# Kernel tuning notes

Measured on AMD Instinct MI355X. Metric: run time of the kernel, lower is better.

Reference implementation:

```python
import jax, jax.numpy as jnp
import numpy as np

B, LT, D, H, DI = 8, 128, 512, 8, 2048
NMEM, LMEM = 1024, 64
DH = D // H
EPS = 1e-5
NEG = -1e9

def _ln(x, g, b):
    mu = x.mean(-1, keepdims=True)
    var = ((x - mu) ** 2).mean(-1, keepdims=True)
    return (x - mu) * jax.lax.rsqrt(var + EPS) * g + b

def _ffn(x, W1, b1, W2, b2):
    # PositionwiseFF with residual=True (dropout=0 / eval)
    return x + jax.nn.relu(x @ W1 + b1) @ W2 + b2

def setup_inputs():
    key = jax.random.key(0)
    ks = jax.random.split(key, 16)
    w = lambda i, shape: jax.random.normal(ks[i], shape, jnp.float32) * 0.02
    return {
        "dec_output": jax.random.normal(ks[0], (B, LT, D), jnp.float32),
        "mem_attn_out": jax.random.normal(ks[1], (B, LT, NMEM + 1), jnp.float32),
        "enc_out_mem": jax.random.normal(ks[2], (NMEM, LMEM, D), jnp.float32),
        "tgt_emb_mem": jax.random.normal(ks[3], (NMEM, LMEM, D), jnp.float32),
        "tgt_mask_mem": jax.random.randint(ks[4], (NMEM, LMEM), 0, 2, jnp.int32),
        "tgt_mask": jax.random.randint(ks[5], (B, LT), 0, 2, jnp.int32),
        "g0": jnp.ones((D,), jnp.float32), "be0": jnp.zeros((D,), jnp.float32),
        "g1": jnp.ones((D,), jnp.float32), "be1": jnp.zeros((D,), jnp.float32),
        "Wq": w(6, (D, D)), "bq": jnp.zeros((D,), jnp.float32),
        "Wk": w(7, (D, D)), "bk": jnp.zeros((D,), jnp.float32),
        "Wv": w(8, (D, D)), "bv": jnp.zeros((D,), jnp.float32),
        "Wo": w(9, (D, D)), "bo": jnp.zeros((D,), jnp.float32),
        "f1W1": w(10, (D, DI)), "f1b1": jnp.zeros((DI,), jnp.float32),
        "f1W2": w(11, (DI, D)), "f1b2": jnp.zeros((D,), jnp.float32),
        "f2W1": w(12, (D, DI)), "f2b1": jnp.zeros((DI,), jnp.float32),
        "f2W2": w(13, (DI, D)), "f2b2": jnp.zeros((D,), jnp.float32),
    }

def reference(dec_output, mem_attn_out, enc_out_mem, tgt_emb_mem, tgt_mask_mem, tgt_mask,
              g0, be0, g1, be1, Wq, bq, Wk, bk, Wv, bv, Wo, bo,
              f1W1, f1b1, f1W2, f1b2, f2W1, f2b1, f2W2, f2b2):
    x = _ln(dec_output, g0, be0)                       # [B,LT,D]
    N = B * LT
    samples = jnp.argmax(mem_attn_out, -1).reshape(N) - 1   # [-1, NMEM-1]
    valid = samples >= 0                               # [N]
    s = jnp.maximum(samples, 0)                        # clamp; masked later
    q = x.reshape(N, 1, D)
    # gather memory per selected query (torch compacts via unique; same math)
    k_in = enc_out_mem[s]                              # [N,LMEM,D]
    v_in = tgt_emb_mem[s]                              # [N,LMEM,D]
    kmask = tgt_mask_mem[s] != 0                       # True = valid key
    # multi-head attention, residual=True
    qh = (q @ Wq + bq).reshape(N, 1, H, DH).transpose(0, 2, 1, 3)     # [N,H,1,DH]
    kh = (k_in @ Wk + bk).reshape(N, LMEM, H, DH).transpose(0, 2, 1, 3)
    vh = (v_in @ Wv + bv).reshape(N, LMEM, H, DH).transpose(0, 2, 1, 3)
    scores = jnp.einsum('nhqd,nhkd->nhqk', qh, kh) / (DH ** 0.5)      # [N,H,1,LMEM]
    scores = jnp.where(kmask[:, None, None, :], scores, NEG)
    attn = jax.nn.softmax(scores, axis=-1)
    ctx = jnp.einsum('nhqk,nhkd->nhqd', attn, vh).transpose(0, 2, 1, 3).reshape(N, 1, D)
    st = q + ctx @ Wo + bo
    st = _ffn(st, f1W1, f1b1, f1W2, f1b2)
    st = _ln(st, g1, be1)
    # scatter back: positions with sample == -1 get zeros
    st = jnp.where(valid[:, None, None], st, 0.0)
    dec = x + st.reshape(B, LT, D)
    dec = _ffn(dec, f2W1, f2b1, f2W2, f2b2)
    return dec
```

## Files before the change

kernel.cpp:

```cpp
#include <hip/hip_runtime.h>
#include <math.h>

#define NQ   1024
#define DIM  512
#define NH   8
#define DHD  64
#define DFF  2048
#define LM   64

typedef __bf16 bf16x8 __attribute__((ext_vector_type(8)));
typedef float  f32x4  __attribute__((ext_vector_type(4)));

__device__ __forceinline__ unsigned short f2bf(float f) {
    unsigned u = __builtin_bit_cast(unsigned, f);
    return (unsigned short)((u + 0x7fffu + ((u >> 16) & 1u)) >> 16);
}
__device__ __forceinline__ float bflo(unsigned p) {
    return __builtin_bit_cast(float, p << 16);
}
__device__ __forceinline__ float bfhi(unsigned p) {
    return __builtin_bit_cast(float, p & 0xffff0000u);
}

__device__ __forceinline__ void gload16(const void* g, void* l) {
    __builtin_amdgcn_global_load_lds(
        (const __attribute__((address_space(1))) unsigned*)g,
        (__attribute__((address_space(3))) unsigned*)l, 16, 0, 0);
}

__device__ __forceinline__ float blk_sum(float v, volatile float* red) {
#pragma unroll
    for (int o = 32; o; o >>= 1) v += __shfl_down(v, o);
    __syncthreads();
    if ((threadIdx.x & 63) == 0) red[threadIdx.x >> 6] = v;
    __syncthreads();
    return red[0] + red[1] + red[2] + red[3];
}

struct PrepPtrs {
    const float* src[8];
    unsigned short* dst[8];
};
__global__ __launch_bounds__(256) void prep_ln0_k(
    PrepPtrs p,
    const float* __restrict__ dec_out, const float* __restrict__ attn_out,
    const float* __restrict__ g, const float* __restrict__ be,
    float* __restrict__ x, unsigned* __restrict__ xb, int* __restrict__ samples)
{
    __shared__ float tile[32][33];
    __shared__ float red[4];
    __shared__ float rv[4]; __shared__ int ri[4];
    const int bid = blockIdx.x;

    if (bid < 5120) {
        int m, lt;
        if (bid < 1024) { m = bid >> 8; lt = bid & 255; }
        else { m = 4 + ((bid - 1024) >> 10); lt = (bid - 1024) & 1023; }
        const int RS = (m < 4) ? 512 : ((m == 5 || m == 7) ? 2048 : 512);
        const int CS = (m < 4) ? 512 : ((m == 5 || m == 7) ? 512 : 2048);
        const int TC = CS >> 5;
        const int tr = lt / TC, tc = lt % TC;
        const float* s = p.src[m];
        unsigned short* d = p.dst[m];
        const int tx = threadIdx.x & 31, ty = threadIdx.x >> 5;
        if (m == 1) {
#pragma unroll
            for (int i = 0; i < 32; i += 8) {
                size_t idx = (size_t)(tr * 32 + ty + i) * CS + tc * 32 + tx;
                d[idx] = f2bf(s[idx]);
            }
        } else {
#pragma unroll
            for (int i = 0; i < 32; i += 8)
                tile[ty + i][tx] = s[(size_t)(tr * 32 + ty + i) * CS + tc * 32 + tx];
            __syncthreads();
#pragma unroll
            for (int i = 0; i < 32; i += 8)
                d[(size_t)(tc * 32 + ty + i) * RS + tr * 32 + tx] = f2bf(tile[tx][ty + i]);
        }
        return;
    }

    const int n = bid - 5120, t = threadIdx.x;
    float2 v = ((const float2*)(dec_out + (size_t)n * DIM))[t];
    float mu  = blk_sum(v.x + v.y, red) * (1.f / DIM);
    float dx = v.x - mu, dy = v.y - mu;
    float var = blk_sum(dx * dx + dy * dy, red) * (1.f / DIM);
    float rs = rsqrtf(var + 1e-5f);
    float2 gg = ((const float2*)g)[t], bb = ((const float2*)be)[t];
    float ox = dx * rs * gg.x + bb.x, oy = dy * rs * gg.y + bb.y;
    ((float2*)(x + (size_t)n * DIM))[t] = make_float2(ox, oy);
    xb[(size_t)n * 256 + t] = (unsigned)f2bf(ox) | ((unsigned)f2bf(oy) << 16);

    const float* ar = attn_out + (size_t)n * 1025;
    float bv = -INFINITY; int bi = 0x7fffffff;
    for (int i = t; i < 1025; i += 256) {
        float val = ar[i];
        if (val > bv || (val == bv && i < bi)) { bv = val; bi = i; }
    }
#pragma unroll
    for (int o = 32; o; o >>= 1) {
        float ov = __shfl_down(bv, o); int oi = __shfl_down(bi, o);
        if (ov > bv || (ov == bv && oi < bi)) { bv = ov; bi = oi; }
    }
    if ((t & 63) == 0) { rv[t >> 6] = bv; ri[t >> 6] = bi; }
    __syncthreads();
    if (t == 0) {
#pragma unroll
        for (int w = 1; w < 4; ++w)
            if (rv[w] > bv || (rv[w] == bv && ri[w] < bi)) { bv = rv[w]; bi = ri[w]; }
        samples[n] = bi - 1;
    }
}

template<bool RELU, bool BIAS, bool RES, bool WF32, bool WBF>
__global__ __launch_bounds__(256) void mfma_gemm(
    const unsigned short* __restrict__ A, const unsigned short* __restrict__ Bt,
    float* __restrict__ Cf, unsigned short* __restrict__ Cb,
    const float* __restrict__ bias, const float* __restrict__ res,
    int K, int lda, int ldb, int ldc,
    int sA, int sB, int sC, int sBias)
{
    __shared__ unsigned short Ab[2][64 * 64];
    __shared__ unsigned short Bb[2][64 * 64];
    const int t = threadIdx.x, lane = t & 63, wid = t >> 6;
    const int bm = blockIdx.y * 64, bn = blockIdx.x * 64, bz = blockIdx.z;
    const unsigned short* Abase = A + (size_t)bz * sA + (size_t)bm * lda;
    const unsigned short* Bbase = Bt + (size_t)bz * sB + (size_t)bn * ldb;

    const int r0 = wid * 16 + (lane >> 3);
    const int cbs = lane & 7;

#define STAGE_T(buf, base, ld, kt)                                              \
    {                                                                           \
        int r_ = r0;                                                            \
        gload16(base + (size_t)r_ * ld + (kt) * 64 + ((cbs ^ (r_ & 7)) << 3),   \
                &buf[(wid * 2 + 0) * 512]);                                     \
        r_ = r0 + 8;                                                            \
        gload16(base + (size_t)r_ * ld + (kt) * 64 + ((cbs ^ (r_ & 7)) << 3),   \
                &buf[(wid * 2 + 1) * 512]);                                     \
    }

    const int lr = lane & 15, lg = lane >> 4;
    const int wr = (wid >> 1) * 32, wc = (wid & 1) * 32;
    const int mA0 = wr + lr, mA1 = wr + 16 + lr;
    const int nB0 = wc + lr, nB1 = wc + 16 + lr;
    f32x4 acc[2][2] = {};

#define COMPUTE(b)                                                              \
    _Pragma("unroll")                                                           \
    for (int kk = 0; kk < 2; ++kk) {                                            \
        const int kb = kk * 4 + lg;                                             \
        bf16x8 a0 = *(const bf16x8*)&Ab[b][mA0 * 64 + ((kb ^ (mA0 & 7)) << 3)]; \
        bf16x8 a1 = *(const bf16x8*)&Ab[b][mA1 * 64 + ((kb ^ (mA1 & 7)) << 3)]; \
        bf16x8 b0 = *(const bf16x8*)&Bb[b][nB0 * 64 + ((kb ^ (nB0 & 7)) << 3)]; \
        bf16x8 b1 = *(const bf16x8*)&Bb[b][nB1 * 64 + ((kb ^ (nB1 & 7)) << 3)]; \
        acc[0][0] = __builtin_amdgcn_mfma_f32_16x16x32_bf16(a0, b0, acc[0][0], 0, 0, 0); \
        acc[0][1] = __builtin_amdgcn_mfma_f32_16x16x32_bf16(a0, b1, acc[0][1], 0, 0, 0); \
        acc[1][0] = __builtin_amdgcn_mfma_f32_16x16x32_bf16(a1, b0, acc[1][0], 0, 0, 0); \
        acc[1][1] = __builtin_amdgcn_mfma_f32_16x16x32_bf16(a1, b1, acc[1][1], 0, 0, 0); \
    }

    STAGE_T(Ab[0], Abase, lda, 0);
    STAGE_T(Bb[0], Bbase, ldb, 0);
    __syncthreads();
    const int NT = K >> 6;
    int cur = 0;
    for (int kt = 0; kt < NT; ++kt) {
        if (kt + 1 < NT) {
            STAGE_T(Ab[cur ^ 1], Abase, lda, kt + 1);
            STAGE_T(Bb[cur ^ 1], Bbase, ldb, kt + 1);
        }
        if (cur == 0) { COMPUTE(0); } else { COMPUTE(1); }
        __syncthreads();
        cur ^= 1;
    }

#pragma unroll
    for (int fm = 0; fm < 2; ++fm)
#pragma unroll
    for (int fn = 0; fn < 2; ++fn) {
        const int col = bn + wc + fn * 16 + lr;
        float bia = BIAS ? bias[bz * sBias + col] : 0.f;
#pragma unroll
        for (int r = 0; r < 4; ++r) {
            const int row = bm + wr + fm * 16 + lg * 4 + r;
            const size_t ci = (size_t)bz * sC + (size_t)row * ldc + col;
            float v = acc[fm][fn][r] + bia;
            if (RES) v += res[(size_t)row * ldc + col];
            if (RELU) v = fmaxf(v, 0.f);
            if (WF32) Cf[ci] = v;
            if (WBF)  Cb[ci] = f2bf(v);
        }
    }
#undef STAGE_T
#undef COMPUTE
}

__global__ __launch_bounds__(256) void attn_scores_k(
    const float* __restrict__ qh, const unsigned short* __restrict__ u_bf,
    const float* __restrict__ enc, const int* __restrict__ samples,
    const float* __restrict__ bk, float* __restrict__ s_part)
{
    __shared__ float Cs_lds[8];
    const int n = blockIdx.x, half = blockIdx.y, t = threadIdx.x;
    const int lane = t & 63, w = t >> 6;
    int s = samples[n]; if (s < 0) s = 0;

    const float4* kb = (const float4*)(enc + (size_t)s * (LM * DIM));
    const int key = w * 16 + (lane & 15);
    const int lg = lane >> 4;
    const int h = lane & 15;
    const int base = key * 128 + half * 64 + lg * 2;
    float4 pf[4][2];
#pragma unroll
    for (int ss = 0; ss < 4; ++ss) {
        pf[ss][0] = kb[base + ss * 8];
        pf[ss][1] = kb[base + ss * 8 + 1];
    }

    if (w == 1) {
        int hq = lane >> 3, j = lane & 7;
        const float4* q4 = (const float4*)(qh + (size_t)n * DIM + hq * 64 + j * 8);
        const float4* b4 = (const float4*)(bk + hq * 64 + j * 8);
        float4 qa = q4[0], qb = q4[1], ba = b4[0], bb = b4[1];
        float c = qa.x * ba.x + qa.y * ba.y + qa.z * ba.z + qa.w * ba.w
                + qb.x * bb.x + qb.y * bb.y + qb.z * bb.z + qb.w * bb.w;
        c += __shfl_xor(c, 1); c += __shfl_xor(c, 2); c += __shfl_xor(c, 4);
        if (j == 0) Cs_lds[hq] = c;
    }

    const unsigned short* ub = u_bf + (size_t)n * 4096 + (size_t)(h & 7) * 512 + half * 256;
    f32x4 acc = {};
#pragma unroll
    for (int step = 0; step < 8; ++step) {
        float4 a0 = pf[step & 3][0], a1 = pf[step & 3][1];
        if (step + 4 < 8) {
            pf[step & 3][0] = kb[base + (step + 4) * 8];
            pf[step & 3][1] = kb[base + (step + 4) * 8 + 1];
        }
        bf16x8 af;
        af[0] = (__bf16)a0.x; af[1] = (__bf16)a0.y;
        af[2] = (__bf16)a0.z; af[3] = (__bf16)a0.w;
        af[4] = (__bf16)a1.x; af[5] = (__bf16)a1.y;
        af[6] = (__bf16)a1.z; af[7] = (__bf16)a1.w;
        bf16x8 bfr = *(const bf16x8*)&ub[(step * 4 + lg) * 8];
        acc = __builtin_amdgcn_mfma_f32_16x16x32_bf16(af, bfr, acc, 0, 0, 0);
    }
    __syncthreads();
    if (h < 8) {
        float cs = (half == 0) ? Cs_lds[h] : 0.f;
        float* sp = s_part + (((size_t)n * 2 + half) * 8 + h) * 64 + w * 16 + lg * 4;
        *(float4*)sp = make_float4(acc[0] + cs, acc[1] + cs, acc[2] + cs, acc[3] + cs);
    }
}

__global__ __launch_bounds__(256) void attn_pv_k(
    const float* __restrict__ s_part, const float* __restrict__ vemb,
    const int* __restrict__ maskmem, const int* __restrict__ samples,
    unsigned* __restrict__ a_bf)
{
    __shared__ float Sp_lds[1024];
    __shared__ uint4 P_lds[64];
    __shared__ float2 Red[8][128];
    __shared__ int Msk_lds[64];
    const int n = blockIdx.x, dh = blockIdx.y, t = threadIdx.x;
    const int lane = t & 63, w = t >> 6;
    int s = samples[n]; if (s < 0) s = 0;

    ((float4*)Sp_lds)[t] = ((const float4*)(s_part + (size_t)n * 1024))[t];
    if (t < 64) Msk_lds[t] = maskmem[(size_t)s * LM + t];
    __syncthreads();

#pragma unroll
    for (int hh = 0; hh < 2; ++hh) {
        const int h = w + hh * 4;
        float sc = (Sp_lds[h * 64 + lane] + Sp_lds[512 + h * 64 + lane]) * 0.125f;
        sc = (Msk_lds[lane] != 0) ? sc : -1e9f;
        float m = sc;
#pragma unroll
        for (int o = 32; o; o >>= 1) m = fmaxf(m, __shfl_xor(m, o));
        float e = __expf(sc - m);
        float su = e;
#pragma unroll
        for (int o = 32; o; o >>= 1) su += __shfl_xor(su, o);
        ((unsigned short*)P_lds)[lane * 8 + h] = f2bf(e / su);
    }
    __syncthreads();

    const int c = t & 127, kh = t >> 7;
    const float2* vb = (const float2*)(vemb + (size_t)s * (LM * DIM)) + dh * 128 + c;
    float2 acc8[8];
#pragma unroll
    for (int hh = 0; hh < 8; ++hh) acc8[hh] = make_float2(0.f, 0.f);
#pragma unroll 8
    for (int i = 0; i < 32; ++i) {
        const int k = kh * 32 + i;
        float2 v = vb[(size_t)k * 256];
        uint4 pr = P_lds[k];
        float p0 = bflo(pr.x), p1 = bfhi(pr.x);
        float p2 = bflo(pr.y), p3 = bfhi(pr.y);
        float p4 = bflo(pr.z), p5 = bfhi(pr.z);
        float p6 = bflo(pr.w), p7 = bfhi(pr.w);
        acc8[0].x = fmaf(p0, v.x, acc8[0].x); acc8[0].y = fmaf(p0, v.y, acc8[0].y);
        acc8[1].x = fmaf(p1, v.x, acc8[1].x); acc8[1].y = fmaf(p1, v.y, acc8[1].y);
        acc8[2].x = fmaf(p2, v.x, acc8[2].x); acc8[2].y = fmaf(p2, v.y, acc8[2].y);
        acc8[3].x = fmaf(p3, v.x, acc8[3].x); acc8[3].y = fmaf(p3, v.y, acc8[3].y);
        acc8[4].x = fmaf(p4, v.x, acc8[4].x); acc8[4].y = fmaf(p4, v.y, acc8[4].y);
        acc8[5].x = fmaf(p5, v.x, acc8[5].x); acc8[5].y = fmaf(p5, v.y, acc8[5].y);
        acc8[6].x = fmaf(p6, v.x, acc8[6].x); acc8[6].y = fmaf(p6, v.y, acc8[6].y);
        acc8[7].x = fmaf(p7, v.x, acc8[7].x); acc8[7].y = fmaf(p7, v.y, acc8[7].y);
    }
    if (kh == 1) {
#pragma unroll
        for (int hh = 0; hh < 8; ++hh) Red[hh][c] = acc8[hh];
    }
    __syncthreads();
    if (kh == 0) {
        unsigned* an = a_bf + (size_t)n * 2048 + dh * 128;
#pragma unroll
        for (int hh = 0; hh < 8; ++hh) {
            float2 r = Red[hh][c];
            float ox = acc8[hh].x + r.x, oy = acc8[hh].y + r.y;
            an[hh * 256 + c] = (unsigned)f2bf(ox) | ((unsigned)f2bf(oy) << 16);
        }
    }
}

__global__ __launch_bounds__(256) void ln1_mask_add_k(
    const float* __restrict__ t1p, const float* __restrict__ st0,
    const float* __restrict__ b2, const float* __restrict__ g,
    const float* __restrict__ be, const int* __restrict__ samples,
    const float* __restrict__ x, float* __restrict__ dec, unsigned* __restrict__ decb)
{
    __shared__ float red[4];
    const int n = blockIdx.x, t = threadIdx.x;
    float2 p0 = ((const float2*)(t1p + (size_t)n * DIM))[t];
    float2 p1 = ((const float2*)(t1p + (size_t)(NQ + n) * DIM))[t];
    float2 s0 = ((const float2*)(st0 + (size_t)n * DIM))[t];
    float2 b2v = ((const float2*)b2)[t];
    float2 v = make_float2(p0.x + p1.x + s0.x + b2v.x, p0.y + p1.y + s0.y + b2v.y);
    float mu  = blk_sum(v.x + v.y, red) * (1.f / DIM);
    float dx = v.x - mu, dy = v.y - mu;
    float var = blk_sum(dx * dx + dy * dy, red) * (1.f / DIM);
    float rs = rsqrtf(var + 1e-5f);
    float2 gg = ((const float2*)g)[t], bb = ((const float2*)be)[t];
    float sx = dx * rs * gg.x + bb.x, sy = dy * rs * gg.y + bb.y;
    if (samples[n] < 0) { sx = 0.f; sy = 0.f; }
    float2 xx = ((const float2*)(x + (size_t)n * DIM))[t];
    float ox = xx.x + sx, oy = xx.y + sy;
    ((float2*)(dec + (size_t)n * DIM))[t] = make_float2(ox, oy);
    decb[(size_t)n * 256 + t] = (unsigned)f2bf(ox) | ((unsigned)f2bf(oy) << 16);
}

extern "C" void kernel_launch(void* const* d_in, const int* in_sizes, int n_in,
                              void* d_out, int out_size, void* d_ws, size_t ws_size,
                              hipStream_t stream)
{
    const float* dec_output = (const float*)d_in[0];
    const float* mem_attn   = (const float*)d_in[1];
    const float* enc_mem    = (const float*)d_in[2];
    const float* temb_mem   = (const float*)d_in[3];
    const int*   mask_mem   = (const int*)d_in[4];
    const float* g0  = (const float*)d_in[6];
    const float* be0 = (const float*)d_in[7];
    const float* g1  = (const float*)d_in[8];
    const float* be1 = (const float*)d_in[9];
    const float* Wq  = (const float*)d_in[10];
    const float* bq  = (const float*)d_in[11];
    const float* Wk  = (const float*)d_in[12];
    const float* bk  = (const float*)d_in[13];
    const float* Wv  = (const float*)d_in[14];
    const float* bv  = (const float*)d_in[15];
    const float* Wo  = (const float*)d_in[16];
    const float* bo  = (const float*)d_in[17];
    const float* f1W1 = (const float*)d_in[18];
    const float* f1b1 = (const float*)d_in[19];
    const float* f1W2 = (const float*)d_in[20];
    const float* f1b2 = (const float*)d_in[21];
    const float* f2W1 = (const float*)d_in[22];
    const float* f2b1 = (const float*)d_in[23];
    const float* f2W2 = (const float*)d_in[24];
    const float* f2b2 = (const float*)d_in[25];
    float* out = (float*)d_out;

    float* ws = (float*)d_ws;
    float*          x_f   = ws + 0;
    unsigned*       x_b   = (unsigned*)(ws + 524288);
    float*          qh_f  = ws + 786432;
    unsigned short* qh_b  = (unsigned short*)(ws + 1310720);
    unsigned short* u_b   = (unsigned short*)(ws + 1572864);
    unsigned short* a_b   = (unsigned short*)(ws + 3670016);
    unsigned short* wqt   = (unsigned short*)(ws + 5767168);
    unsigned short* wkc   = (unsigned short*)(ws + 5898240);
    unsigned short* wvt   = (unsigned short*)(ws + 6029312);
    unsigned short* wot   = (unsigned short*)(ws + 6160384);
    unsigned short* f1w1t = (unsigned short*)(ws + 6291456);
    unsigned short* f1w2t = (unsigned short*)(ws + 6815744);
    unsigned short* f2w1t = (unsigned short*)(ws + 7340032);
    unsigned short* f2w2t = (unsigned short*)(ws + 7864320);
    int*            smp   = (int*)(ws + 8388608);
    float*          s_prt = ws + 8392704;
    float*          t1p_f = ws + 9441280;
    float*          st0_f = (float*)u_b + 0;
    unsigned short* st0_b = (unsigned short*)((float*)u_b + 524288);
    float*          dec_f = (float*)u_b + 1310720;
    unsigned*       dec_b = (unsigned*)((float*)u_b + 1835008);
    unsigned short* h1_b  = a_b;
    unsigned short* h2_b  = (unsigned short*)((float*)a_b + 1048576);

    PrepPtrs pp;
    pp.src[0] = Wq;   pp.dst[0] = wqt;
    pp.src[1] = Wk;   pp.dst[1] = wkc;
    pp.src[2] = Wv;   pp.dst[2] = wvt;
    pp.src[3] = Wo;   pp.dst[3] = wot;
    pp.src[4] = f1W1; pp.dst[4] = f1w1t;
    pp.src[5] = f1W2; pp.dst[5] = f1w2t;
    pp.src[6] = f2W1; pp.dst[6] = f2w1t;
    pp.src[7] = f2W2; pp.dst[7] = f2w2t;
    prep_ln0_k<<<5120 + NQ, 256, 0, stream>>>(pp, dec_output, mem_attn, g0, be0,
                                              x_f, x_b, smp);
    mfma_gemm<false, true, false, true, true><<<dim3(8, 16, 1), 256, 0, stream>>>(
        (const unsigned short*)x_b, wqt, qh_f, qh_b, bq, nullptr,
        DIM, DIM, DIM, DIM, 0, 0, 0, 0);
    mfma_gemm<false, false, false, false, true><<<dim3(8, 16, NH), 256, 0, stream>>>(
        qh_b, wkc, nullptr, u_b, nullptr, nullptr,
        DHD, DIM, DIM, NH * DIM, DHD, DHD, DIM, 0);
    attn_scores_k<<<dim3(NQ, 2), 256, 0, stream>>>(qh_f, u_b, enc_mem, smp, bk, s_prt);
    attn_pv_k<<<dim3(NQ, 2), 256, 0, stream>>>(s_prt, temb_mem, mask_mem, smp,
                                               (unsigned*)a_b);
    mfma_gemm<false, true, false, false, true><<<dim3(1, 16, NH), 256, 0, stream>>>(
        a_b, wvt, nullptr, qh_b, bv, nullptr,
        DIM, NH * DIM, DIM, DIM, DIM, DHD * DIM, DHD, DHD);
    mfma_gemm<false, true, true, true, true><<<dim3(8, 16, 1), 256, 0, stream>>>(
        qh_b, wot, st0_f, st0_b, bo, x_f, DIM, DIM, DIM, DIM, 0, 0, 0, 0);
    mfma_gemm<true, true, false, false, true><<<dim3(32, 16, 1), 256, 0, stream>>>(
        st0_b, f1w1t, nullptr, h1_b, f1b1, nullptr, DIM, DIM, DIM, DFF, 0, 0, 0, 0);
    mfma_gemm<false, false, false, true, false><<<dim3(8, 16, 2), 256, 0, stream>>>(
        h1_b, f1w2t, t1p_f, nullptr, nullptr, nullptr,
        1024, DFF, DFF, DIM, 1024, 1024, NQ * DIM, 0);
    ln1_mask_add_k<<<NQ, 256, 0, stream>>>(t1p_f, st0_f, f1b2, g1, be1, smp,
                                           x_f, dec_f, dec_b);
    mfma_gemm<true, true, false, false, true><<<dim3(32, 16, 1), 256, 0, stream>>>(
        (const unsigned short*)dec_b, f2w1t, nullptr, h2_b, f2b1, nullptr,
        DIM, DIM, DIM, DFF, 0, 0, 0, 0);
    mfma_gemm<false, true, true, true, false><<<dim3(8, 16, 1), 256, 0, stream>>>(
        h2_b, f2w2t, out, nullptr, f2b2, dec_f, DFF, DFF, DFF, DIM, 0, 0, 0, 0);

    (void)in_sizes; (void)n_in; (void)out_size; (void)ws_size;
}
```

Measured before the change: 157.2 us.

## Fold Wq·Wk and Wv·Wo into per-head combined weights, split-K FFN down-projection

Precomputes per-head fused weight products Wq_h·Wk_hᵀ and Wv_h·Wo_h (plus folded biases) in the prep kernel. The query projection and the q→key-space GEMM collapse into one batched GEMM from x, and the V and O projections collapse into one batched GEMM followed by a new merge kernel that sums the eight head partials. The FFN1 down-projection split-K rises from 2 to 4. This removes two dependent GEMM launches and the per-row bias dot product in the scores kernel. In exchange it adds costly FP32 SIMT weight-product work in prep, more FLOPs per fused GEMM, and larger partial buffers to write and reduce.

```diff
diff --git a/kernel.cpp b/kernel.cpp
--- a/kernel.cpp
+++ b/kernel.cpp
@@ -37,79 +37,144 @@
     return red[0] + red[1] + red[2] + red[3];
 }
 
-struct PrepPtrs {
-    const float* src[8];
-    unsigned short* dst[8];
+struct PrepArgs {
+    const float *Wq, *Wk, *Wv, *Wo, *bq, *bv, *bo;
+    unsigned short *wqk, *wvo;
+    float *bqk, *bvo;
+    const float* fsrc[4];
+    unsigned short* fdst[4];
+    const float *dec_out, *attn_out, *g0, *be0;
+    float* x; unsigned* xb; int* samples;
 };
-__global__ __launch_bounds__(256) void prep_ln0_k(
-    PrepPtrs p,
-    const float* __restrict__ dec_out, const float* __restrict__ attn_out,
-    const float* __restrict__ g, const float* __restrict__ be,
-    float* __restrict__ x, unsigned* __restrict__ xb, int* __restrict__ samples)
-{
+__global__ __launch_bounds__(256) void prep_ln0_k(PrepArgs P) {
+    __shared__ float ldsA[64][65];
+    __shared__ float ldsB[64][65];
     __shared__ float tile[32][33];
     __shared__ float red[4];
     __shared__ float rv[4]; __shared__ int ri[4];
-    const int bid = blockIdx.x;
-
+    const int bid = blockIdx.x, t = threadIdx.x;
+
+    if (bid < 1024) {
+        const int mat = bid >> 9, rem = bid & 511;
+        const int h = rem >> 6, tl = rem & 63;
+        const int c0 = (tl >> 3) * 64, k0 = (tl & 7) * 64;
+        const float* Bsrc = mat ? P.Wv : P.Wq;
+        for (int idx = t; idx < 1024; idx += 256) {
+            int k = idx >> 4, j4 = idx & 15;
+            float4 v = *(const float4*)&Bsrc[(size_t)(k0 + k) * 512 + h * 64 + j4 * 4];
+            ldsB[k][j4 * 4 + 0] = v.x; ldsB[k][j4 * 4 + 1] = v.y;
+            ldsB[k][j4 * 4 + 2] = v.z; ldsB[k][j4 * 4 + 3] = v.w;
+        }
+        if (mat == 0) {
+            for (int idx = t; idx < 1024; idx += 256) {
+                int c = idx >> 4, j4 = idx & 15;
+                float4 v = *(const float4*)&P.Wk[(size_t)(c0 + c) * 512 + h * 64 + j4 * 4];
+                ldsA[c][j4 * 4 + 0] = v.x; ldsA[c][j4 * 4 + 1] = v.y;
+                ldsA[c][j4 * 4 + 2] = v.z; ldsA[c][j4 * 4 + 3] = v.w;
+            }
+        } else {
+            for (int idx = t; idx < 1024; idx += 256) {
+                int j = idx >> 4, c4 = idx & 15;
+                float4 v = *(const float4*)&P.Wo[(size_t)(h * 64 + j) * 512 + c0 + c4 * 4];
+                ldsA[c4 * 4 + 0][j] = v.x; ldsA[c4 * 4 + 1][j] = v.y;
+                ldsA[c4 * 4 + 2][j] = v.z; ldsA[c4 * 4 + 3][j] = v.w;
+            }
+        }
+        __syncthreads();
+        const int ty = t >> 4, tx = t & 15;
+        float acc[4][4] = {};
+#pragma unroll 8
+        for (int j = 0; j < 64; ++j) {
+            float a0 = ldsA[ty * 4 + 0][j], a1 = ldsA[ty * 4 + 1][j];
+            float a2 = ldsA[ty * 4 + 2][j], a3 = ldsA[ty * 4 + 3][j];
+            float b0 = ldsB[tx * 4 + 0][j], b1 = ldsB[tx * 4 + 1][j];
+            float b2 = ldsB[tx * 4 + 2][j], b3 = ldsB[tx * 4 + 3][j];
+            acc[0][0] = fmaf(a0, b0, acc[0][0]); acc[0][1] = fmaf(a0, b1, acc[0][1]);
+            acc[0][2] = fmaf(a0, b2, acc[0][2]); acc[0][3] = fmaf(a0, b3, acc[0][3]);
+            acc[1][0] = fmaf(a1, b0, acc[1][0]); acc[1][1] = fmaf(a1, b1, acc[1][1]);
+            acc[1][2] = fmaf(a1, b2, acc[1][2]); acc[1][3] = fmaf(a1, b3, acc[1][3]);
+            acc[2][0] = fmaf(a2, b0, acc[2][0]); acc[2][1] = fmaf(a2, b1, acc[2][1]);
+            acc[2][2] = fmaf(a2, b2, acc[2][2]); acc[2][3] = fmaf(a2, b3, acc[2][3]);
+            acc[3][0] = fmaf(a3, b0, acc[3][0]); acc[3][1] = fmaf(a3, b1, acc[3][1]);
+            acc[3][2] = fmaf(a3, b2, acc[3][2]); acc[3][3] = fmaf(a3, b3, acc[3][3]);
+        }
+        unsigned short* dst = mat ? P.wvo : P.wqk;
+#pragma unroll
+        for (int i = 0; i < 4; ++i) {
+            size_t o = ((size_t)h * 512 + c0 + ty * 4 + i) * 512 + k0 + tx * 4;
+            dst[o + 0] = f2bf(acc[i][0]); dst[o + 1] = f2bf(acc[i][1]);
+            dst[o + 2] = f2bf(acc[i][2]); dst[o + 3] = f2bf(acc[i][3]);
+        }
+        return;
+    }
     if (bid < 5120) {
-        int m, lt;
-        if (bid < 1024) { m = bid >> 8; lt = bid & 255; }
-        else { m = 4 + ((bid - 1024) >> 10); lt = (bid - 1024) & 1023; }
-        const int RS = (m < 4) ? 512 : ((m == 5 || m == 7) ? 2048 : 512);
-        const int CS = (m < 4) ? 512 : ((m == 5 || m == 7) ? 512 : 2048);
+        const int f = (bid - 1024) >> 10, lt = (bid - 1024) & 1023;
+        const int RS = (f & 1) ? 2048 : 512;
+        const int CS = (f & 1) ? 512 : 2048;
         const int TC = CS >> 5;
         const int tr = lt / TC, tc = lt % TC;
-        const float* s = p.src[m];
-        unsigned short* d = p.dst[m];
-        const int tx = threadIdx.x & 31, ty = threadIdx.x >> 5;
-        if (m == 1) {
-#pragma unroll
-            for (int i = 0; i < 32; i += 8) {
-                size_t idx = (size_t)(tr * 32 + ty + i) * CS + tc * 32 + tx;
-                d[idx] = f2bf(s[idx]);
-            }
-        } else {
-#pragma unroll
-            for (int i = 0; i < 32; i += 8)
-                tile[ty + i][tx] = s[(size_t)(tr * 32 + ty + i) * CS + tc * 32 + tx];
-            __syncthreads();
-#pragma unroll
-            for (int i = 0; i < 32; i += 8)
-                d[(size_t)(tc * 32 + ty + i) * RS + tr * 32 + tx] = f2bf(tile[tx][ty + i]);
-        }
+        const float* s = P.fsrc[f];
+        unsigned short* d = P.fdst[f];
+        const int tx = t & 31, ty = t >> 5;
+#pragma unroll
+        for (int i = 0; i < 32; i += 8)
+            tile[ty + i][tx] = s[(size_t)(tr * 32 + ty + i) * CS + tc * 32 + tx];
+        __syncthreads();
+#pragma unroll
+        for (int i = 0; i < 32; i += 8)
+            d[(size_t)(tc * 32 + ty + i) * RS + tr * 32 + tx] = f2bf(tile[tx][ty + i]);
         return;
     }
-
-    const int n = bid - 5120, t = threadIdx.x;
-    float2 v = ((const float2*)(dec_out + (size_t)n * DIM))[t];
+    if (bid < 5128) {
+        const int h = bid - 5120;
+#pragma unroll
+        for (int rep = 0; rep < 2; ++rep) {
+            int d = t + rep * 256;
+            float a = 0.f;
+            for (int j = 0; j < 64; ++j)
+                a += P.bq[h * 64 + j] * P.Wk[(size_t)d * 512 + h * 64 + j];
+            P.bqk[h * 512 + d] = a;
+        }
+        return;
+    }
+    if (bid < 5130) {
+        const int c = (bid - 5128) * 256 + t;
+        float a = P.bo[c];
+        for (int d = 0; d < 512; ++d) a += P.bv[d] * P.Wo[(size_t)d * 512 + c];
+        P.bvo[c] = a;
+        return;
+    }
+    if (bid < 5136) return;
+
+    const int n = bid - 5136;
+    float2 v = ((const float2*)(P.dec_out + (size_t)n * DIM))[t];
     float mu  = blk_sum(v.x + v.y, red) * (1.f / DIM);
     float dx = v.x - mu, dy = v.y - mu;
     float var = blk_sum(dx * dx + dy * dy, red) * (1.f / DIM);
     float rs = rsqrtf(var + 1e-5f);
-    float2 gg = ((const float2*)g)[t], bb = ((const float2*)be)[t];
+    float2 gg = ((const float2*)P.g0)[t], bb = ((const float2*)P.be0)[t];
     float ox = dx * rs * gg.x + bb.x, oy = dy * rs * gg.y + bb.y;
-    ((float2*)(x + (size_t)n * DIM))[t] = make_float2(ox, oy);
-    xb[(size_t)n * 256 + t] = (unsigned)f2bf(ox) | ((unsigned)f2bf(oy) << 16);
-
-    const float* ar = attn_out + (size_t)n * 1025;
-    float bv = -INFINITY; int bi = 0x7fffffff;
+    ((float2*)(P.x + (size_t)n * DIM))[t] = make_float2(ox, oy);
+    P.xb[(size_t)n * 256 + t] = (unsigned)f2bf(ox) | ((unsigned)f2bf(oy) << 16);
+
+    const float* ar = P.attn_out + (size_t)n * 1025;
+    float bvx = -INFINITY; int bi = 0x7fffffff;
     for (int i = t; i < 1025; i += 256) {
         float val = ar[i];
-        if (val > bv || (val == bv && i < bi)) { bv = val; bi = i; }
+        if (val > bvx || (val == bvx && i < bi)) { bvx = val; bi = i; }
     }
 #pragma unroll
     for (int o = 32; o; o >>= 1) {
-        float ov = __shfl_down(bv, o); int oi = __shfl_down(bi, o);
-        if (ov > bv || (ov == bv && oi < bi)) { bv = ov; bi = oi; }
-    }
-    if ((t & 63) == 0) { rv[t >> 6] = bv; ri[t >> 6] = bi; }
+        float ov = __shfl_down(bvx, o); int oi = __shfl_down(bi, o);
+        if (ov > bvx || (ov == bvx && oi < bi)) { bvx = ov; bi = oi; }
+    }
+    if ((t & 63) == 0) { rv[t >> 6] = bvx; ri[t >> 6] = bi; }
     __syncthreads();
     if (t == 0) {
 #pragma unroll
         for (int w = 1; w < 4; ++w)
-            if (rv[w] > bv || (rv[w] == bv && ri[w] < bi)) { bv = rv[w]; bi = ri[w]; }
-        samples[n] = bi - 1;
+            if (rv[w] > bvx || (rv[w] == bvx && ri[w] < bi)) { bvx = rv[w]; bi = ri[w]; }
+        P.samples[n] = bi - 1;
     }
 }
 
@@ -198,11 +263,9 @@
 }
 
 __global__ __launch_bounds__(256) void attn_scores_k(
-    const float* __restrict__ qh, const unsigned short* __restrict__ u_bf,
-    const float* __restrict__ enc, const int* __restrict__ samples,
-    const float* __restrict__ bk, float* __restrict__ s_part)
+    const unsigned short* __restrict__ u_bf, const float* __restrict__ enc,
+    const int* __restrict__ samples, float* __restrict__ s_part)
 {
-    __shared__ float Cs_lds[8];
     const int n = blockIdx.x, half = blockIdx.y, t = threadIdx.x;
     const int lane = t & 63, w = t >> 6;
     int s = samples[n]; if (s < 0) s = 0;
@@ -217,17 +280,6 @@
     for (int ss = 0; ss < 4; ++ss) {
         pf[ss][0] = kb[base + ss * 8];
         pf[ss][1] = kb[base + ss * 8 + 1];
-    }
-
-    if (w == 1) {
-        int hq = lane >> 3, j = lane & 7;
-        const float4* q4 = (const float4*)(qh + (size_t)n * DIM + hq * 64 + j * 8);
-        const float4* b4 = (const float4*)(bk + hq * 64 + j * 8);
-        float4 qa = q4[0], qb = q4[1], ba = b4[0], bb = b4[1];
-        float c = qa.x * ba.x + qa.y * ba.y + qa.z * ba.z + qa.w * ba.w
-                + qb.x * bb.x + qb.y * bb.y + qb.z * bb.z + qb.w * bb.w;
-        c += __shfl_xor(c, 1); c += __shfl_xor(c, 2); c += __shfl_xor(c, 4);
-        if (j == 0) Cs_lds[hq] = c;
     }
 
     const unsigned short* ub = u_bf + (size_t)n * 4096 + (size_t)(h & 7) * 512 + half * 256;
@@ -247,11 +299,9 @@
         bf16x8 bfr = *(const bf16x8*)&ub[(step * 4 + lg) * 8];
         acc = __builtin_amdgcn_mfma_f32_16x16x32_bf16(af, bfr, acc, 0, 0, 0);
     }
-    __syncthreads();
     if (h < 8) {
-        float cs = (half == 0) ? Cs_lds[h] : 0.f;
         float* sp = s_part + (((size_t)n * 2 + half) * 8 + h) * 64 + w * 16 + lg * 4;
-        *(float4*)sp = make_float4(acc[0] + cs, acc[1] + cs, acc[2] + cs, acc[3] + cs);
+        *(float4*)sp = make_float4(acc[0], acc[1], acc[2], acc[3]);
     }
 }
 
@@ -327,6 +377,25 @@
     }
 }
 
+__global__ __launch_bounds__(256) void merge_st0_k(
+    const float* __restrict__ stov, const float* __restrict__ x,
+    const float* __restrict__ bvo,
+    float* __restrict__ st0f, unsigned* __restrict__ st0b)
+{
+    const int n = blockIdx.x, t = threadIdx.x;
+    const size_t off = (size_t)n * DIM + t * 2;
+    float2 acc = *(const float2*)&x[off];
+    float2 bv2 = ((const float2*)bvo)[t];
+    acc.x += bv2.x; acc.y += bv2.y;
+#pragma unroll
+    for (int z = 0; z < 8; ++z) {
+        float2 p = *(const float2*)&stov[(size_t)z * (NQ * DIM) + off];
+        acc.x += p.x; acc.y += p.y;
+    }
+    *(float2*)&st0f[off] = acc;
+    st0b[(size_t)n * 256 + t] = (unsigned)f2bf(acc.x) | ((unsigned)f2bf(acc.y) << 16);
+}
+
 __global__ __launch_bounds__(256) void ln1_mask_add_k(
     const float* __restrict__ t1p, const float* __restrict__ st0,
     const float* __restrict__ b2, const float* __restrict__ g,
@@ -335,11 +404,15 @@
 {
     __shared__ float red[4];
     const int n = blockIdx.x, t = threadIdx.x;
-    float2 p0 = ((const float2*)(t1p + (size_t)n * DIM))[t];
-    float2 p1 = ((const float2*)(t1p + (size_t)(NQ + n) * DIM))[t];
-    float2 s0 = ((const float2*)(st0 + (size_t)n * DIM))[t];
+    const size_t off = (size_t)n * DIM + t * 2;
+    float2 s0 = *(const float2*)&st0[off];
     float2 b2v = ((const float2*)b2)[t];
-    float2 v = make_float2(p0.x + p1.x + s0.x + b2v.x, p0.y + p1.y + s0.y + b2v.y);
+    float2 v = make_float2(s0.x + b2v.x, s0.y + b2v.y);
+#pragma unroll
+    for (int z = 0; z < 4; ++z) {
+        float2 p = *(const float2*)&t1p[(size_t)z * (NQ * DIM) + off];
+        v.x += p.x; v.y += p.y;
+    }
     float mu  = blk_sum(v.x + v.y, red) * (1.f / DIM);
     float dx = v.x - mu, dy = v.y - mu;
     float var = blk_sum(dx * dx + dy * dy, red) * (1.f / DIM);
@@ -347,9 +420,9 @@
     float2 gg = ((const float2*)g)[t], bb = ((const float2*)be)[t];
     float sx = dx * rs * gg.x + bb.x, sy = dy * rs * gg.y + bb.y;
     if (samples[n] < 0) { sx = 0.f; sy = 0.f; }
-    float2 xx = ((const float2*)(x + (size_t)n * DIM))[t];
+    float2 xx = *(const float2*)&x[off];
     float ox = xx.x + sx, oy = xx.y + sy;
-    ((float2*)(dec + (size_t)n * DIM))[t] = make_float2(ox, oy);
+    *(float2*)&dec[off] = make_float2(ox, oy);
     decb[(size_t)n * 256 + t] = (unsigned)f2bf(ox) | ((unsigned)f2bf(oy) << 16);
 }
 
@@ -369,7 +442,6 @@
     const float* Wq  = (const float*)d_in[10];
     const float* bq  = (const float*)d_in[11];
     const float* Wk  = (const float*)d_in[12];
-    const float* bk  = (const float*)d_in[13];
     const float* Wv  = (const float*)d_in[14];
     const float* bv  = (const float*)d_in[15];
     const float* Wo  = (const float*)d_in[16];
@@ -387,58 +459,53 @@
     float* ws = (float*)d_ws;
     float*          x_f   = ws + 0;
     unsigned*       x_b   = (unsigned*)(ws + 524288);
-    float*          qh_f  = ws + 786432;
-    unsigned short* qh_b  = (unsigned short*)(ws + 1310720);
-    unsigned short* u_b   = (unsigned short*)(ws + 1572864);
-    unsigned short* a_b   = (unsigned short*)(ws + 3670016);
-    unsigned short* wqt   = (unsigned short*)(ws + 5767168);
-    unsigned short* wkc   = (unsigned short*)(ws + 5898240);
-    unsigned short* wvt   = (unsigned short*)(ws + 6029312);
-    unsigned short* wot   = (unsigned short*)(ws + 6160384);
-    unsigned short* f1w1t = (unsigned short*)(ws + 6291456);
-    unsigned short* f1w2t = (unsigned short*)(ws + 6815744);
-    unsigned short* f2w1t = (unsigned short*)(ws + 7340032);
-    unsigned short* f2w2t = (unsigned short*)(ws + 7864320);
-    int*            smp   = (int*)(ws + 8388608);
-    float*          s_prt = ws + 8392704;
-    float*          t1p_f = ws + 9441280;
+    unsigned short* u_b   = (unsigned short*)(ws + 786432);
+    unsigned short* a_b   = (unsigned short*)(ws + 2883584);
+    float*          s_prt = ws + 4980736;
+    unsigned short* wqk   = (unsigned short*)(ws + 6029312);
+    unsigned short* wvo   = (unsigned short*)(ws + 7077888);
+    unsigned short* f1w1t = (unsigned short*)(ws + 8126464);
+    unsigned short* f1w2t = (unsigned short*)(ws + 8650752);
+    unsigned short* f2w1t = (unsigned short*)(ws + 9175040);
+    unsigned short* f2w2t = (unsigned short*)(ws + 9699328);
+    float*          bqk   = ws + 10223616;
+    float*          bvo   = ws + 10227712;
+    int*            smp   = (int*)(ws + 10228224);
+    float*          stov  = ws + 10229248;
+    float*          t1p_f = ws + 14423552;
     float*          st0_f = (float*)u_b + 0;
     unsigned short* st0_b = (unsigned short*)((float*)u_b + 524288);
-    float*          dec_f = (float*)u_b + 1310720;
-    unsigned*       dec_b = (unsigned*)((float*)u_b + 1835008);
+    float*          dec_f = (float*)u_b + 655360;
+    unsigned*       dec_b = (unsigned*)((float*)u_b + 1179648);
     unsigned short* h1_b  = a_b;
     unsigned short* h2_b  = (unsigned short*)((float*)a_b + 1048576);
 
-    PrepPtrs pp;
-    pp.src[0] = Wq;   pp.dst[0] = wqt;
-    pp.src[1] = Wk;   pp.dst[1] = wkc;
-    pp.src[2] = Wv;   pp.dst[2] = wvt;
-    pp.src[3] = Wo;   pp.dst[3] = wot;
-    pp.src[4] = f1W1; pp.dst[4] = f1w1t;
-    pp.src[5] = f1W2; pp.dst[5] = f1w2t;
-    pp.src[6] = f2W1; pp.dst[6] = f2w1t;
-    pp.src[7] = f2W2; pp.dst[7] = f2w2t;
-    prep_ln0_k<<<5120 + NQ, 256, 0, stream>>>(pp, dec_output, mem_attn, g0, be0,
-                                              x_f, x_b, smp);
-    mfma_gemm<false, true, false, true, true><<<dim3(8, 16, 1), 256, 0, stream>>>(
-        (const unsigned short*)x_b, wqt, qh_f, qh_b, bq, nullptr,
-        DIM, DIM, DIM, DIM, 0, 0, 0, 0);
-    mfma_gemm<false, false, false, false, true><<<dim3(8, 16, NH), 256, 0, stream>>>(
-        qh_b, wkc, nullptr, u_b, nullptr, nullptr,
-        DHD, DIM, DIM, NH * DIM, DHD, DHD, DIM, 0);
-    attn_scores_k<<<dim3(NQ, 2), 256, 0, stream>>>(qh_f, u_b, enc_mem, smp, bk, s_prt);
+    PrepArgs P;
+    P.Wq = Wq; P.Wk = Wk; P.Wv = Wv; P.Wo = Wo; P.bq = bq; P.bv = bv; P.bo = bo;
+    P.wqk = wqk; P.wvo = wvo; P.bqk = bqk; P.bvo = bvo;
+    P.fsrc[0] = f1W1; P.fdst[0] = f1w1t;
+    P.fsrc[1] = f1W2; P.fdst[1] = f1w2t;
+    P.fsrc[2] = f2W1; P.fdst[2] = f2w1t;
+    P.fsrc[3] = f2W2; P.fdst[3] = f2w2t;
+    P.dec_out = dec_output; P.attn_out = mem_attn; P.g0 = g0; P.be0 = be0;
+    P.x = x_f; P.xb = x_b; P.samples = smp;
+
+    prep_ln0_k<<<6160, 256, 0, stream>>>(P);
+    mfma_gemm<false, true, false, false, true><<<dim3(8, 16, NH), 256, 0, stream>>>(
+        (const unsigned short*)x_b, wqk, nullptr, u_b, bqk, nullptr,
+        DIM, DIM, DIM, NH * DIM, 0, DIM * DIM, DIM, DIM);
+    attn_scores_k<<<dim3(NQ, 2), 256, 0, stream>>>(u_b, enc_mem, smp, s_prt);
     attn_pv_k<<<dim3(NQ, 2), 256, 0, stream>>>(s_prt, temb_mem, mask_mem, smp,
                                                (unsigned*)a_b);
-    mfma_gemm<false, true, false, false, true><<<dim3(1, 16, NH), 256, 0, stream>>>(
-        a_b, wvt, nullptr, qh_b, bv, nullptr,
-        DIM, NH * DIM, DIM, DIM, DIM, DHD * DIM, DHD, DHD);
-    mfma_gemm<false, true, true, true, true><<<dim3(8, 16, 1), 256, 0, stream>>>(
-        qh_b, wot, st0_f, st0_b, bo, x_f, DIM, DIM, DIM, DIM, 0, 0, 0, 0);
+    mfma_gemm<false, false, false, true, false><<<dim3(8, 16, NH), 256, 0, stream>>>(
+        a_b, wvo, stov, nullptr, nullptr, nullptr,
+        DIM, NH * DIM, DIM, DIM, DIM, DIM * DIM, NQ * DIM, 0);
+    merge_st0_k<<<NQ, 256, 0, stream>>>(stov, x_f, bvo, st0_f, (unsigned*)st0_b);
     mfma_gemm<true, true, false, false, true><<<dim3(32, 16, 1), 256, 0, stream>>>(
         st0_b, f1w1t, nullptr, h1_b, f1b1, nullptr, DIM, DIM, DIM, DFF, 0, 0, 0, 0);
-    mfma_gemm<false, false, false, true, false><<<dim3(8, 16, 2), 256, 0, stream>>>(
+    mfma_gemm<false, false, false, true, false><<<dim3(8, 16, 4), 256, 0, stream>>>(
         h1_b, f1w2t, t1p_f, nullptr, nullptr, nullptr,
-        1024, DFF, DFF, DIM, 1024, 1024, NQ * DIM, 0);
+        DIM, DFF, DFF, DIM, DIM, DIM, NQ * DIM, 0);
     ln1_mask_add_k<<<NQ, 256, 0, stream>>>(t1p_f, st0_f, f1b2, g1, be1, smp,
                                            x_f, dec_f, dec_b);
     mfma_gemm<true, true, false, false, true><<<dim3(32, 16, 1), 256, 0, stream>>>(
```

Measured after the change: 176.8 us. +12.5%, slower.

## Split attention kernels four ways, drop softmax-invariant key bias, swizzle GEMM tiles

Applied to the files above, without the earlier changes.

The score and PV attention kernels now split each query's work into four slices instead of two. This doubles the grid, shortens each block's serial loop, and removes the in-loop prefetch and a barrier. The q·bk term is dropped because it adds the same constant to every key score within a head, which softmax ignores; that also removes the fp32 copy of Q and its write. GEMM blocks are remapped with an 8-way interleave over tile indices, meant to group neighbouring tiles on the same XCD for cache reuse. The workspace is re-laid out for the larger score-partial buffer, at the cost of an extra partial-sum read in the PV kernel.

```diff
diff --git a/kernel.cpp b/kernel.cpp
--- a/kernel.cpp
+++ b/kernel.cpp
@@ -124,7 +124,11 @@
     __shared__ unsigned short Ab[2][64 * 64];
     __shared__ unsigned short Bb[2][64 * 64];
     const int t = threadIdx.x, lane = t & 63, wid = t >> 6;
-    const int bm = blockIdx.y * 64, bn = blockIdx.x * 64, bz = blockIdx.z;
+    const int nx = gridDim.x;
+    const int fid = blockIdx.y * nx + blockIdx.x;
+    const int cpx = (nx * gridDim.y) >> 3;
+    const int f2 = (fid & 7) * cpx + (fid >> 3);
+    const int bn = (f2 % nx) * 64, bm = (f2 / nx) * 64, bz = blockIdx.z;
     const unsigned short* Abase = A + (size_t)bz * sA + (size_t)bm * lda;
     const unsigned short* Bbase = Bt + (size_t)bz * sB + (size_t)bn * ldb;
 
@@ -198,12 +202,10 @@
 }
 
 __global__ __launch_bounds__(256) void attn_scores_k(
-    const float* __restrict__ qh, const unsigned short* __restrict__ u_bf,
-    const float* __restrict__ enc, const int* __restrict__ samples,
-    const float* __restrict__ bk, float* __restrict__ s_part)
-{
-    __shared__ float Cs_lds[8];
-    const int n = blockIdx.x, half = blockIdx.y, t = threadIdx.x;
+    const unsigned short* __restrict__ u_bf, const float* __restrict__ enc,
+    const int* __restrict__ samples, float* __restrict__ s_part)
+{
+    const int n = blockIdx.x, q = blockIdx.y, t = threadIdx.x;
     const int lane = t & 63, w = t >> 6;
     int s = samples[n]; if (s < 0) s = 0;
 
@@ -211,7 +213,7 @@
     const int key = w * 16 + (lane & 15);
     const int lg = lane >> 4;
     const int h = lane & 15;
-    const int base = key * 128 + half * 64 + lg * 2;
+    const int base = key * 128 + q * 32 + lg * 2;
     float4 pf[4][2];
 #pragma unroll
     for (int ss = 0; ss < 4; ++ss) {
@@ -219,26 +221,11 @@
         pf[ss][1] = kb[base + ss * 8 + 1];
     }
 
-    if (w == 1) {
-        int hq = lane >> 3, j = lane & 7;
-        const float4* q4 = (const float4*)(qh + (size_t)n * DIM + hq * 64 + j * 8);
-        const float4* b4 = (const float4*)(bk + hq * 64 + j * 8);
-        float4 qa = q4[0], qb = q4[1], ba = b4[0], bb = b4[1];
-        float c = qa.x * ba.x + qa.y * ba.y + qa.z * ba.z + qa.w * ba.w
-                + qb.x * bb.x + qb.y * bb.y + qb.z * bb.z + qb.w * bb.w;
-        c += __shfl_xor(c, 1); c += __shfl_xor(c, 2); c += __shfl_xor(c, 4);
-        if (j == 0) Cs_lds[hq] = c;
-    }
-
-    const unsigned short* ub = u_bf + (size_t)n * 4096 + (size_t)(h & 7) * 512 + half * 256;
+    const unsigned short* ub = u_bf + (size_t)n * 4096 + (size_t)(h & 7) * 512 + q * 128;
     f32x4 acc = {};
 #pragma unroll
-    for (int step = 0; step < 8; ++step) {
-        float4 a0 = pf[step & 3][0], a1 = pf[step & 3][1];
-        if (step + 4 < 8) {
-            pf[step & 3][0] = kb[base + (step + 4) * 8];
-            pf[step & 3][1] = kb[base + (step + 4) * 8 + 1];
-        }
+    for (int step = 0; step < 4; ++step) {
+        float4 a0 = pf[step][0], a1 = pf[step][1];
         bf16x8 af;
         af[0] = (__bf16)a0.x; af[1] = (__bf16)a0.y;
         af[2] = (__bf16)a0.z; af[3] = (__bf16)a0.w;
@@ -247,11 +234,9 @@
         bf16x8 bfr = *(const bf16x8*)&ub[(step * 4 + lg) * 8];
         acc = __builtin_amdgcn_mfma_f32_16x16x32_bf16(af, bfr, acc, 0, 0, 0);
     }
-    __syncthreads();
     if (h < 8) {
-        float cs = (half == 0) ? Cs_lds[h] : 0.f;
-        float* sp = s_part + (((size_t)n * 2 + half) * 8 + h) * 64 + w * 16 + lg * 4;
-        *(float4*)sp = make_float4(acc[0] + cs, acc[1] + cs, acc[2] + cs, acc[3] + cs);
+        float* sp = s_part + (((size_t)n * 4 + q) * 8 + h) * 64 + w * 16 + lg * 4;
+        *(float4*)sp = make_float4(acc[0], acc[1], acc[2], acc[3]);
     }
 }
 
@@ -260,22 +245,24 @@
     const int* __restrict__ maskmem, const int* __restrict__ samples,
     unsigned* __restrict__ a_bf)
 {
-    __shared__ float Sp_lds[1024];
+    __shared__ float Sp_lds[2048];
     __shared__ uint4 P_lds[64];
-    __shared__ float2 Red[8][128];
+    __shared__ float2 Red[3][8][64];
     __shared__ int Msk_lds[64];
-    const int n = blockIdx.x, dh = blockIdx.y, t = threadIdx.x;
+    const int n = blockIdx.x, dq = blockIdx.y, t = threadIdx.x;
     const int lane = t & 63, w = t >> 6;
     int s = samples[n]; if (s < 0) s = 0;
 
-    ((float4*)Sp_lds)[t] = ((const float4*)(s_part + (size_t)n * 1024))[t];
+    ((float4*)Sp_lds)[t]       = ((const float4*)(s_part + (size_t)n * 2048))[t];
+    ((float4*)Sp_lds)[t + 256] = ((const float4*)(s_part + (size_t)n * 2048))[t + 256];
     if (t < 64) Msk_lds[t] = maskmem[(size_t)s * LM + t];
     __syncthreads();
 
 #pragma unroll
     for (int hh = 0; hh < 2; ++hh) {
         const int h = w + hh * 4;
-        float sc = (Sp_lds[h * 64 + lane] + Sp_lds[512 + h * 64 + lane]) * 0.125f;
+        float sc = (Sp_lds[h * 64 + lane] + Sp_lds[512 + h * 64 + lane]
+                  + Sp_lds[1024 + h * 64 + lane] + Sp_lds[1536 + h * 64 + lane]) * 0.125f;
         sc = (Msk_lds[lane] != 0) ? sc : -1e9f;
         float m = sc;
 #pragma unroll
@@ -288,14 +275,14 @@
     }
     __syncthreads();
 
-    const int c = t & 127, kh = t >> 7;
-    const float2* vb = (const float2*)(vemb + (size_t)s * (LM * DIM)) + dh * 128 + c;
+    const int c = t & 63, kh = t >> 6;
+    const float2* vb = (const float2*)(vemb + (size_t)s * (LM * DIM)) + dq * 64 + c;
     float2 acc8[8];
 #pragma unroll
     for (int hh = 0; hh < 8; ++hh) acc8[hh] = make_float2(0.f, 0.f);
 #pragma unroll 8
-    for (int i = 0; i < 32; ++i) {
-        const int k = kh * 32 + i;
+    for (int i = 0; i < 16; ++i) {
+        const int k = kh * 16 + i;
         float2 v = vb[(size_t)k * 256];
         uint4 pr = P_lds[k];
         float p0 = bflo(pr.x), p1 = bfhi(pr.x);
@@ -311,17 +298,18 @@
         acc8[6].x = fmaf(p6, v.x, acc8[6].x); acc8[6].y = fmaf(p6, v.y, acc8[6].y);
         acc8[7].x = fmaf(p7, v.x, acc8[7].x); acc8[7].y = fmaf(p7, v.y, acc8[7].y);
     }
-    if (kh == 1) {
-#pragma unroll
-        for (int hh = 0; hh < 8; ++hh) Red[hh][c] = acc8[hh];
+    if (kh > 0) {
+#pragma unroll
+        for (int hh = 0; hh < 8; ++hh) Red[kh - 1][hh][c] = acc8[hh];
     }
     __syncthreads();
     if (kh == 0) {
-        unsigned* an = a_bf + (size_t)n * 2048 + dh * 128;
+        unsigned* an = a_bf + (size_t)n * 2048 + dq * 64;
 #pragma unroll
         for (int hh = 0; hh < 8; ++hh) {
-            float2 r = Red[hh][c];
-            float ox = acc8[hh].x + r.x, oy = acc8[hh].y + r.y;
+            float2 r0 = Red[0][hh][c], r1 = Red[1][hh][c], r2 = Red[2][hh][c];
+            float ox = acc8[hh].x + r0.x + r1.x + r2.x;
+            float oy = acc8[hh].y + r0.y + r1.y + r2.y;
             an[hh * 256 + c] = (unsigned)f2bf(ox) | ((unsigned)f2bf(oy) << 16);
         }
     }
@@ -335,9 +323,10 @@
 {
     __shared__ float red[4];
     const int n = blockIdx.x, t = threadIdx.x;
-    float2 p0 = ((const float2*)(t1p + (size_t)n * DIM))[t];
-    float2 p1 = ((const float2*)(t1p + (size_t)(NQ + n) * DIM))[t];
-    float2 s0 = ((const float2*)(st0 + (size_t)n * DIM))[t];
+    const size_t off = (size_t)n * DIM + t * 2;
+    float2 p0 = *(const float2*)&t1p[off];
+    float2 p1 = *(const float2*)&t1p[(size_t)NQ * DIM + off];
+    float2 s0 = *(const float2*)&st0[off];
     float2 b2v = ((const float2*)b2)[t];
     float2 v = make_float2(p0.x + p1.x + s0.x + b2v.x, p0.y + p1.y + s0.y + b2v.y);
     float mu  = blk_sum(v.x + v.y, red) * (1.f / DIM);
@@ -347,9 +336,9 @@
     float2 gg = ((const float2*)g)[t], bb = ((const float2*)be)[t];
     float sx = dx * rs * gg.x + bb.x, sy = dy * rs * gg.y + bb.y;
     if (samples[n] < 0) { sx = 0.f; sy = 0.f; }
-    float2 xx = ((const float2*)(x + (size_t)n * DIM))[t];
+    float2 xx = *(const float2*)&x[off];
     float ox = xx.x + sx, oy = xx.y + sy;
-    ((float2*)(dec + (size_t)n * DIM))[t] = make_float2(ox, oy);
+    *(float2*)&dec[off] = make_float2(ox, oy);
     decb[(size_t)n * 256 + t] = (unsigned)f2bf(ox) | ((unsigned)f2bf(oy) << 16);
 }
 
@@ -369,7 +358,6 @@
     const float* Wq  = (const float*)d_in[10];
     const float* bq  = (const float*)d_in[11];
     const float* Wk  = (const float*)d_in[12];
-    const float* bk  = (const float*)d_in[13];
     const float* Wv  = (const float*)d_in[14];
     const float* bv  = (const float*)d_in[15];
     const float* Wo  = (const float*)d_in[16];
@@ -387,25 +375,24 @@
     float* ws = (float*)d_ws;
     float*          x_f   = ws + 0;
     unsigned*       x_b   = (unsigned*)(ws + 524288);
-    float*          qh_f  = ws + 786432;
-    unsigned short* qh_b  = (unsigned short*)(ws + 1310720);
-    unsigned short* u_b   = (unsigned short*)(ws + 1572864);
-    unsigned short* a_b   = (unsigned short*)(ws + 3670016);
-    unsigned short* wqt   = (unsigned short*)(ws + 5767168);
-    unsigned short* wkc   = (unsigned short*)(ws + 5898240);
-    unsigned short* wvt   = (unsigned short*)(ws + 6029312);
-    unsigned short* wot   = (unsigned short*)(ws + 6160384);
-    unsigned short* f1w1t = (unsigned short*)(ws + 6291456);
-    unsigned short* f1w2t = (unsigned short*)(ws + 6815744);
-    unsigned short* f2w1t = (unsigned short*)(ws + 7340032);
-    unsigned short* f2w2t = (unsigned short*)(ws + 7864320);
-    int*            smp   = (int*)(ws + 8388608);
-    float*          s_prt = ws + 8392704;
-    float*          t1p_f = ws + 9441280;
+    unsigned short* qh_b  = (unsigned short*)(ws + 786432);
+    unsigned short* u_b   = (unsigned short*)(ws + 1048576);
+    unsigned short* a_b   = (unsigned short*)(ws + 3145728);
+    float*          s_prt = ws + 5242880;
+    unsigned short* wqt   = (unsigned short*)(ws + 7340032);
+    unsigned short* wkc   = (unsigned short*)(ws + 7471104);
+    unsigned short* wvt   = (unsigned short*)(ws + 7602176);
+    unsigned short* wot   = (unsigned short*)(ws + 7733248);
+    unsigned short* f1w1t = (unsigned short*)(ws + 7864320);
+    unsigned short* f1w2t = (unsigned short*)(ws + 8388608);
+    unsigned short* f2w1t = (unsigned short*)(ws + 8912896);
+    unsigned short* f2w2t = (unsigned short*)(ws + 9437184);
+    int*            smp   = (int*)(ws + 9961472);
+    float*          t1p_f = ws + 9962496;
     float*          st0_f = (float*)u_b + 0;
     unsigned short* st0_b = (unsigned short*)((float*)u_b + 524288);
-    float*          dec_f = (float*)u_b + 1310720;
-    unsigned*       dec_b = (unsigned*)((float*)u_b + 1835008);
+    float*          dec_f = (float*)u_b + 655360;
+    unsigned*       dec_b = (unsigned*)((float*)u_b + 1179648);
     unsigned short* h1_b  = a_b;
     unsigned short* h2_b  = (unsigned short*)((float*)a_b + 1048576);
 
@@ -420,14 +407,14 @@
     pp.src[7] = f2W2; pp.dst[7] = f2w2t;
     prep_ln0_k<<<5120 + NQ, 256, 0, stream>>>(pp, dec_output, mem_attn, g0, be0,
                                               x_f, x_b, smp);
-    mfma_gemm<false, true, false, true, true><<<dim3(8, 16, 1), 256, 0, stream>>>(
-        (const unsigned short*)x_b, wqt, qh_f, qh_b, bq, nullptr,
+    mfma_gemm<false, true, false, false, true><<<dim3(8, 16, 1), 256, 0, stream>>>(
+        (const unsigned short*)x_b, wqt, nullptr, qh_b, bq, nullptr,
         DIM, DIM, DIM, DIM, 0, 0, 0, 0);
     mfma_gemm<false, false, false, false, true><<<dim3(8, 16, NH), 256, 0, stream>>>(
         qh_b, wkc, nullptr, u_b, nullptr, nullptr,
         DHD, DIM, DIM, NH * DIM, DHD, DHD, DIM, 0);
-    attn_scores_k<<<dim3(NQ, 2), 256, 0, stream>>>(qh_f, u_b, enc_mem, smp, bk, s_prt);
-    attn_pv_k<<<dim3(NQ, 2), 256, 0, stream>>>(s_prt, temb_mem, mask_mem, smp,
+    attn_scores_k<<<dim3(NQ, 4), 256, 0, stream>>>(u_b, enc_mem, smp, s_prt);
+    attn_pv_k<<<dim3(NQ, 4), 256, 0, stream>>>(s_prt, temb_mem, mask_mem, smp,
                                                (unsigned*)a_b);
     mfma_gemm<false, true, false, false, true><<<dim3(1, 16, NH), 256, 0, stream>>>(
         a_b, wvt, nullptr, qh_b, bv, nullptr,
```

After: 156.7 us. No clear change (-0.3%).
